# Performance work log

Hardware: AMD Instinct MI355X
Metric: run time of the kernel (lower is better)

Reference implementation:

```python
import jax, jax.numpy as jnp
import numpy as np

N_FILES = 256      # number of files (segments)
LINES = 128        # lines per file
T = N_FILES * LINES  # total lines = 32768
D_ENC = 768        # CodeBERT hidden size
HID = 256          # GCN hidden_dim
SD = 128           # shared_dim
PD = 128           # private_dim
WINDOW = 2         # line-graph window
S_AM = 30.0        # AM-Softmax scale
M_AM = 0.35        # AM-Softmax margin


def _build_edges():
    # build_line_graph: connect lines within a file at offsets 1..WINDOW, both directions
    idx = np.arange(T)
    srcs, dsts = [], []
    for off in range(1, WINDOW + 1):
        m = (idx % LINES) + off < LINES  # j stays inside the same file
        i = idx[m]; j = i + off
        srcs += [i, j]; dsts += [j, i]
    return np.stack([np.concatenate(srcs), np.concatenate(dsts)]).astype(np.int32)


def setup_inputs() -> dict:
    key = jax.random.key(0)
    ks = jax.random.split(key, 18)
    std = 0.02
    inp = {
        "line_emb": jax.random.normal(ks[0], (T, D_ENC), jnp.float32),
        "W1": jax.random.normal(ks[1], (D_ENC, HID), jnp.float32) * std,
        "b1": jnp.zeros((HID,), jnp.float32),
        "W2": jax.random.normal(ks[2], (HID, HID), jnp.float32) * std,
        "b2": jnp.zeros((HID,), jnp.float32),
        "attn_w": jax.random.normal(ks[3], (HID, 1), jnp.float32) * std,
        "attn_b": jnp.zeros((1,), jnp.float32),
        "Ws": jax.random.normal(ks[4], (HID, SD), jnp.float32) * std,
        "bs": jnp.zeros((SD,), jnp.float32),
        "Wp": jax.random.normal(ks[5], (HID, PD), jnp.float32) * std,
        "bp": jnp.zeros((PD,), jnp.float32),
        "cls_w": jax.random.normal(ks[6], (SD, 2), jnp.float32) * std,
        "Wd1": jax.random.normal(ks[7], (SD, SD), jnp.float32) * std,
        "bd1": jnp.zeros((SD,), jnp.float32),
        "Wd2": jax.random.normal(ks[8], (SD, 2), jnp.float32) * std,
        "bd2": jnp.zeros((2,), jnp.float32),
        "line_ptr": jnp.arange(0, T + 1, LINES, dtype=jnp.int32),
        "edge_index": jnp.asarray(_build_edges()),
        "file_labels": jax.random.randint(ks[9], (N_FILES,), 0, 2, jnp.int32),
    }
    return inp


def _l2norm(x):
    return x / jnp.maximum(jnp.linalg.norm(x, axis=1, keepdims=True), 1e-12)


def _gcn(x, W, b, src, dst, n):
    sl = jnp.arange(n, dtype=src.dtype)
    src = jnp.concatenate([src, sl]); dst = jnp.concatenate([dst, sl])
    deg = jax.ops.segment_sum(jnp.ones_like(src, jnp.float32), dst, num_segments=n)
    norm = jax.lax.rsqrt(deg[src] * deg[dst])  # [E+n]
    h = x @ W                                   # [n, out]
    msg = h[src] * norm[:, None]
    return jax.ops.segment_sum(msg, dst, num_segments=n) + b


def reference(line_emb, W1, b1, W2, b2, attn_w, attn_b, Ws, bs, Wp, bp,
              cls_w, Wd1, bd1, Wd2, bd2, line_ptr, edge_index, file_labels):
    n = line_emb.shape[0]
    n_files = line_ptr.shape[0] - 1
    src, dst = edge_index[0], edge_index[1]

    h = jax.nn.relu(_gcn(line_emb, W1, b1, src, dst, n))
    h = _gcn(h, W2, b2, src, dst, n)               # [T, HID]

    # ragged per-file softmax attention pooling
    seg = jnp.searchsorted(line_ptr, jnp.arange(n, dtype=line_ptr.dtype), side="right") - 1
    logits = (h @ attn_w).squeeze(-1) + attn_b[0]  # [T]
    seg_max = jax.ops.segment_max(logits, seg, num_segments=n_files)
    e = jnp.exp(logits - seg_max[seg])
    denom = jax.ops.segment_sum(e, seg, num_segments=n_files)
    att_weights = e / denom[seg]
    h_file = jax.ops.segment_sum(att_weights[:, None] * h, seg, num_segments=n_files)  # [N, HID]

    # disentangle heads
    z_shared = h_file @ Ws + bs
    z_private = h_file @ Wp + bp

    # AM-Softmax classifier (labels given -> subtract margin on true class)
    cos = _l2norm(z_shared) @ (cls_w / jnp.maximum(jnp.linalg.norm(cls_w, axis=0, keepdims=True), 1e-12))
    onehot = jax.nn.one_hot(file_labels, 2, dtype=cos.dtype)
    logits_cls = S_AM * (cos - M_AM * onehot)

    # orthogonality loss
    corr = _l2norm(z_shared).T @ _l2norm(z_private)
    ortho = jnp.linalg.norm(corr)

    # domain discriminator (GRL is identity in forward)
    domain_logits = jax.nn.relu(z_shared @ Wd1 + bd1) @ Wd2 + bd2

    return (logits_cls, h_file, z_shared, z_private, att_weights, domain_logits, ortho)
```

## Files before the change

kernel.cpp:

```cpp
#include <hip/hip_runtime.h>


typedef __attribute__((ext_vector_type(8))) short bf16x8;
typedef __attribute__((ext_vector_type(4))) short bf16x4;
typedef __attribute__((ext_vector_type(4))) float f32x4;
typedef __attribute__((ext_vector_type(8))) float f32x8;

__device__ __forceinline__ unsigned short f2bf(float f) {
  union { float f; unsigned int i; } v; v.f = f;
  unsigned int r = v.i + 0x7FFFu + ((v.i >> 16) & 1u);
  return (unsigned short)(r >> 16);
}
__device__ __forceinline__ int degf(int p) {
  return 5 - (p < 2 ? 2 - p : 0) - (p > 125 ? p - 125 : 0);
}

__global__ void cvt_transpose_tiled(const float* __restrict__ src,
                                    unsigned short* __restrict__ dst, int R, int C) {
  __shared__ float tile[32][33];
  int bx = blockIdx.x * 32, by = blockIdx.y * 32;
  int tx = threadIdx.x, ty = threadIdx.y;
#pragma unroll
  for (int j = 0; j < 32; j += 8)
    tile[ty + j][tx] = src[(by + ty + j) * C + bx + tx];
  __syncthreads();
#pragma unroll
  for (int j = 0; j < 32; j += 8)
    dst[(bx + ty + j) * R + by + tx] = f2bf(tile[tx][ty + j]);
}

__global__ __launch_bounds__(1024) void fused_gcn1(const float* __restrict__ A,
                                                   const unsigned short* __restrict__ Bt,
                                                   const float* __restrict__ bias,
                                                   unsigned short* __restrict__ G1) {
  __shared__ __align__(16) char lds[131072];
  unsigned short* sA = (unsigned short*)lds;
  unsigned short* sB = (unsigned short*)(lds + 32768);
  float* hL = (float*)lds;
  const int t = threadIdx.x;
  const int wave = t >> 6, lane = t & 63;
  const int wr = wave >> 2, wc = wave & 3;
  const long rowA = (long)blockIdx.x * 128;

  f32x4 acc[2][4];
#pragma unroll
  for (int m = 0; m < 2; ++m)
#pragma unroll
    for (int n = 0; n < 4; ++n) acc[m][n] = (f32x4)0.0f;

  const int arow = t >> 3, acol = (t & 7) * 8;
  const int aswz = arow * 64 + (acol ^ ((arow & 7) << 3));
  const int NKT = 12;
  f32x8 areg;

#define ISSUE_A1(kt) areg = *(const f32x8*)&A[(rowA + arow) * 768 + (kt) * 64 + acol]
#define WRITE_A1(buf) { unsigned short u[8];                                      \
    _Pragma("unroll") for (int j = 0; j < 8; ++j) u[j] = f2bf(areg[j]);           \
    *(bf16x8*)&sA[(buf) * 8192 + aswz] = *(bf16x8*)u; }
#define ISSUE_B1(kt, buf) _Pragma("unroll") for (int it = 0; it < 2; ++it) {      \
    int flat = (it * 1024 + t) * 8;                                               \
    int n = flat >> 6, k = flat & 63;                                             \
    const unsigned short* g = Bt + n * 768 + (kt) * 64 + (k ^ ((n & 7) << 3));    \
    __builtin_amdgcn_global_load_lds(                                             \
        (const __attribute__((address_space(1))) unsigned int*)g,                 \
        (__attribute__((address_space(3))) unsigned int*)                         \
            &sB[(buf) * 16384 + (it * 16 + wave) * 512], 16, 0, 0); }

  ISSUE_A1(0); ISSUE_B1(0, 0); WRITE_A1(0);
  __syncthreads();
  for (int kt = 0; kt < NKT; ++kt) {
    const int cur = kt & 1, nxt = cur ^ 1;
    if (kt + 1 < NKT) { ISSUE_A1(kt + 1); ISSUE_B1(kt + 1, nxt); }
#pragma unroll
    for (int kk = 0; kk < 2; ++kk) {
      const int kb = kk * 32 + (lane >> 4) * 8;
      bf16x8 af[2], bfr[4];
#pragma unroll
      for (int m = 0; m < 2; ++m) {
        int r = wr * 32 + m * 16 + (lane & 15);
        af[m] = *(const bf16x8*)&sA[cur * 8192 + r * 64 + (kb ^ ((r & 7) << 3))];
      }
#pragma unroll
      for (int n = 0; n < 4; ++n) {
        int r = wc * 64 + n * 16 + (lane & 15);
        bfr[n] = *(const bf16x8*)&sB[cur * 16384 + r * 64 + (kb ^ ((r & 7) << 3))];
      }
#pragma unroll
      for (int m = 0; m < 2; ++m)
#pragma unroll
        for (int n = 0; n < 4; ++n)
          acc[m][n] = __builtin_amdgcn_mfma_f32_16x16x32_bf16(af[m], bfr[n], acc[m][n], 0, 0, 0);
    }
    if (kt + 1 < NKT) WRITE_A1(nxt);
    __syncthreads();
  }
#pragma unroll
  for (int m = 0; m < 2; ++m)
#pragma unroll
    for (int n = 0; n < 4; ++n) {
      int r = wr * 32 + m * 16 + (lane >> 4) * 4;
      int c = wc * 64 + n * 16 + (lane & 15);
#pragma unroll
      for (int j = 0; j < 4; ++j) hL[(r + j) * 256 + c] = acc[m][n][j];
    }
  __syncthreads();
#pragma unroll
  for (int it = 0; it < 8; ++it) {
    int g = it * 1024 + t;
    int l = g >> 6, c0 = (g & 63) * 4;
    int dl = degf(l);
    f32x4 s = (f32x4)0.0f;
#pragma unroll
    for (int o = -2; o <= 2; ++o) {
      int q = l + o;
      if (q < 0 || q > 127) continue;
      float w = __frsqrt_rn((float)(dl * degf(q)));
      s += w * *(const f32x4*)&hL[q * 256 + c0];
    }
    f32x4 b = *(const f32x4*)&bias[c0];
    unsigned short o4[4];
#pragma unroll
    for (int j = 0; j < 4; ++j) o4[j] = f2bf(fmaxf(s[j] + b[j], 0.f));
    *(bf16x4*)&G1[(rowA + l) * 256 + c0] = *(bf16x4*)o4;
  }
#undef ISSUE_A1
#undef WRITE_A1
#undef ISSUE_B1
}

__global__ __launch_bounds__(1024) void fused_gcn2(const unsigned short* __restrict__ A,
                                                   const unsigned short* __restrict__ Bt,
                                                   const float* __restrict__ bias,
                                                   const float* __restrict__ attn_w,
                                                   const float* __restrict__ attn_b,
                                                   float* __restrict__ hf_ws,
                                                   float* __restrict__ out) {
  __shared__ __align__(16) char lds[131072];
  unsigned short* sA = (unsigned short*)lds;
  unsigned short* sB = (unsigned short*)(lds + 32768);
  float* hL = (float*)lds;
  __shared__ float awS[256];
  __shared__ float lgS[128];
  __shared__ float red[64];
  __shared__ float psum[4 * 256];
  const int t = threadIdx.x;
  const int wave = t >> 6, lane = t & 63;
  const int wr = wave >> 2, wc = wave & 3;
  const int file = blockIdx.x;
  const long rowA = (long)file * 128;

  if (t < 256) awS[t] = attn_w[t];

  f32x4 acc[2][4];
#pragma unroll
  for (int m = 0; m < 2; ++m)
#pragma unroll
    for (int n = 0; n < 4; ++n) acc[m][n] = (f32x4)0.0f;

  const int NKT = 4;

#define ISSUE_A2(kt, buf) {                                                       \
    int flat = t * 8;                                                             \
    int r = flat >> 6, k = flat & 63;                                             \
    const unsigned short* g = A + (rowA + r) * 256 + (kt) * 64 + (k ^ ((r & 7) << 3)); \
    __builtin_amdgcn_global_load_lds(                                             \
        (const __attribute__((address_space(1))) unsigned int*)g,                 \
        (__attribute__((address_space(3))) unsigned int*)                         \
            &sA[(buf) * 8192 + wave * 512], 16, 0, 0); }
#define ISSUE_B2(kt, buf) _Pragma("unroll") for (int it = 0; it < 2; ++it) {      \
    int flat = (it * 1024 + t) * 8;                                               \
    int n = flat >> 6, k = flat & 63;                                             \
    const unsigned short* g = Bt + n * 256 + (kt) * 64 + (k ^ ((n & 7) << 3));    \
    __builtin_amdgcn_global_load_lds(                                             \
        (const __attribute__((address_space(1))) unsigned int*)g,                 \
        (__attribute__((address_space(3))) unsigned int*)                         \
            &sB[(buf) * 16384 + (it * 16 + wave) * 512], 16, 0, 0); }

  ISSUE_A2(0, 0); ISSUE_B2(0, 0);
  __syncthreads();
  for (int kt = 0; kt < NKT; ++kt) {
    const int cur = kt & 1, nxt = cur ^ 1;
    if (kt + 1 < NKT) { ISSUE_A2(kt + 1, nxt); ISSUE_B2(kt + 1, nxt); }
#pragma unroll
    for (int kk = 0; kk < 2; ++kk) {
      const int kb = kk * 32 + (lane >> 4) * 8;
      bf16x8 af[2], bfr[4];
#pragma unroll
      for (int m = 0; m < 2; ++m) {
        int r = wr * 32 + m * 16 + (lane & 15);
        af[m] = *(const bf16x8*)&sA[cur * 8192 + r * 64 + (kb ^ ((r & 7) << 3))];
      }
#pragma unroll
      for (int n = 0; n < 4; ++n) {
        int r = wc * 64 + n * 16 + (lane & 15);
        bfr[n] = *(const bf16x8*)&sB[cur * 16384 + r * 64 + (kb ^ ((r & 7) << 3))];
      }
#pragma unroll
      for (int m = 0; m < 2; ++m)
#pragma unroll
        for (int n = 0; n < 4; ++n)
          acc[m][n] = __builtin_amdgcn_mfma_f32_16x16x32_bf16(af[m], bfr[n], acc[m][n], 0, 0, 0);
    }
    __syncthreads();
  }
#pragma unroll
  for (int m = 0; m < 2; ++m)
#pragma unroll
    for (int n = 0; n < 4; ++n) {
      int r = wr * 32 + m * 16 + (lane >> 4) * 4;
      int c = wc * 64 + n * 16 + (lane & 15);
#pragma unroll
      for (int j = 0; j < 4; ++j) hL[(r + j) * 256 + c] = acc[m][n][j];
    }
  __syncthreads();
  f32x4 st[2];
#pragma unroll
  for (int it = 0; it < 2; ++it) {
    int g = it * 1024 + t;
    int l = g >> 6, c0 = (g & 63) * 4;
    int dl = degf(l);
    f32x4 s = (f32x4)0.0f;
#pragma unroll
    for (int o = -2; o <= 2; ++o) {
      int q = l + o;
      if (q < 0 || q > 127) continue;
      float w = __frsqrt_rn((float)(dl * degf(q)));
      s += w * *(const f32x4*)&hL[q * 256 + c0];
    }
    f32x4 b = *(const f32x4*)&bias[c0];
    st[it] = s + b;
  }
  __syncthreads();
#pragma unroll
  for (int it = 0; it < 2; ++it) {
    int g = it * 1024 + t;
    int l = g >> 6, c0 = (g & 63) * 4;
    *(f32x4*)&hL[l * 256 + c0] = st[it];
  }
  __syncthreads();
  {
    int l = t >> 3, p = t & 7;
    float part = 0.f;
#pragma unroll 4
    for (int j = 0; j < 32; ++j) {
      int c = p * 32 + ((j + 4 * p + l) & 31);
      part += hL[l * 256 + c] * awS[c];
    }
    part += __shfl_xor(part, 1);
    part += __shfl_xor(part, 2);
    part += __shfl_xor(part, 4);
    if (p == 0) lgS[l] = part + attn_b[0];
  }
  __syncthreads();
  if (t < 64) red[t] = fmaxf(lgS[t], lgS[t + 64]);
  __syncthreads();
  for (int s = 32; s > 0; s >>= 1) {
    if (t < s) red[t] = fmaxf(red[t], red[t + s]);
    __syncthreads();
  }
  float mx = red[0];
  __syncthreads();
  if (t < 128) lgS[t] = expf(lgS[t] - mx);
  __syncthreads();
  if (t < 64) red[t] = lgS[t] + lgS[t + 64];
  __syncthreads();
  for (int s = 32; s > 0; s >>= 1) {
    if (t < s) red[t] += red[t + s];
    __syncthreads();
  }
  float dn = red[0];
  __syncthreads();
  if (t < 128) {
    float w = lgS[t] / dn;
    lgS[t] = w;
    out[131584 + file * 128 + t] = w;
  }
  __syncthreads();
  {
    int c = t & 255, grp = t >> 8;
    float s = 0.f;
    for (int l = grp * 32; l < grp * 32 + 32; ++l) s += lgS[l] * hL[l * 256 + c];
    psum[grp * 256 + c] = s;
  }
  __syncthreads();
  if (t < 256) {
    float tot = psum[t] + psum[256 + t] + psum[512 + t] + psum[768 + t];
    hf_ws[file * 256 + t] = tot;
    out[512 + file * 256 + t] = tot;
  }
#undef ISSUE_A2
#undef ISSUE_B2
}

__global__ __launch_bounds__(128) void head_kernel(const float* __restrict__ hf_ws,
    const float* __restrict__ Ws, const float* __restrict__ bs,
    const float* __restrict__ Wp, const float* __restrict__ bp,
    const float* __restrict__ cls_w, const int* __restrict__ labels,
    const float* __restrict__ Wd1, const float* __restrict__ bd1,
    const float* __restrict__ Wd2, const float* __restrict__ bd2,
    float* __restrict__ zsn_ws, float* __restrict__ zpn_ws,
    float* __restrict__ out) {
  const int f = blockIdx.x, j = threadIdx.x;
  __shared__ float hf[256];
  __shared__ float zsS[128];
  __shared__ float red[128];
  hf[j] = hf_ws[f * 256 + j];
  hf[j + 128] = hf_ws[f * 256 + 128 + j];
  __syncthreads();
  float zs = bs[j], zp = bp[j];
  for (int c = 0; c < 256; ++c) {
    float hv = hf[c];
    zs += hv * Ws[c * 128 + j];
    zp += hv * Wp[c * 128 + j];
  }
  out[66048 + f * 128 + j] = zs;
  out[98816 + f * 128 + j] = zp;
  zsS[j] = zs;
  red[j] = zs * zs; __syncthreads();
  for (int s = 64; s > 0; s >>= 1) { if (j < s) red[j] += red[j + s]; __syncthreads(); }
  float ns = sqrtf(red[0]); __syncthreads();
  float zsn = zs / fmaxf(ns, 1e-12f);
  zsn_ws[f * 128 + j] = zsn;
  red[j] = zp * zp; __syncthreads();
  for (int s = 64; s > 0; s >>= 1) { if (j < s) red[j] += red[j + s]; __syncthreads(); }
  float npn = sqrtf(red[0]); __syncthreads();
  zpn_ws[f * 128 + j] = zp / fmaxf(npn, 1e-12f);
  float c0 = 0.f, c1 = 0.f;
#pragma unroll
  for (int k = 0; k < 2; ++k) {
    float cw = cls_w[j * 2 + k];
    red[j] = zsn * cw; __syncthreads();
    for (int s = 64; s > 0; s >>= 1) { if (j < s) red[j] += red[j + s]; __syncthreads(); }
    float dk = red[0]; __syncthreads();
    red[j] = cw * cw; __syncthreads();
    for (int s = 64; s > 0; s >>= 1) { if (j < s) red[j] += red[j + s]; __syncthreads(); }
    float nk = sqrtf(red[0]); __syncthreads();
    float cosv = dk / fmaxf(nk, 1e-12f);
    if (k == 0) c0 = cosv; else c1 = cosv;
  }
  if (j < 2) {
    int lab = labels[f];
    float cv = (j == 0) ? c0 : c1;
    out[f * 2 + j] = 30.0f * (cv - 0.35f * (lab == j ? 1.f : 0.f));
  }
  float dd = bd1[j];
  for (int a = 0; a < 128; ++a) dd += zsS[a] * Wd1[a * 128 + j];
  dd = fmaxf(dd, 0.f);
#pragma unroll
  for (int k = 0; k < 2; ++k) {
    red[j] = dd * Wd2[j * 2 + k]; __syncthreads();
    for (int s = 64; s > 0; s >>= 1) { if (j < s) red[j] += red[j + s]; __syncthreads(); }
    if (j == 0) out[164352 + f * 2 + k] = red[0] + bd2[k];
    __syncthreads();
  }
}

__global__ __launch_bounds__(128) void ortho_partial(const float* __restrict__ zsn,
                                                     const float* __restrict__ zpn,
                                                     float* __restrict__ partial) {
  const int a = blockIdx.x, b = threadIdx.x;
  float s = 0.f;
  for (int f = 0; f < 256; ++f) s += zsn[f * 128 + a] * zpn[f * 128 + b];
  __shared__ float red[128];
  red[b] = s * s; __syncthreads();
  for (int st = 64; st > 0; st >>= 1) { if (b < st) red[b] += red[b + st]; __syncthreads(); }
  if (b == 0) partial[a] = red[0];
}

__global__ __launch_bounds__(128) void ortho_final(const float* __restrict__ partial,
                                                   float* __restrict__ out) {
  const int t = threadIdx.x;
  __shared__ float red[128];
  red[t] = partial[t]; __syncthreads();
  for (int st = 64; st > 0; st >>= 1) { if (t < st) red[t] += red[t + st]; __syncthreads(); }
  if (t == 0) out[164864] = sqrtf(red[0]);
}

extern "C" void kernel_launch(void* const* d_in, const int* in_sizes, int n_in,
                              void* d_out, int out_size, void* d_ws, size_t ws_size,
                              hipStream_t stream) {
  const float* line_emb = (const float*)d_in[0];
  const float* W1     = (const float*)d_in[1];
  const float* b1     = (const float*)d_in[2];
  const float* W2     = (const float*)d_in[3];
  const float* b2     = (const float*)d_in[4];
  const float* attn_w = (const float*)d_in[5];
  const float* attn_b = (const float*)d_in[6];
  const float* Ws     = (const float*)d_in[7];
  const float* bs     = (const float*)d_in[8];
  const float* Wp     = (const float*)d_in[9];
  const float* bp     = (const float*)d_in[10];
  const float* cls_w  = (const float*)d_in[11];
  const float* Wd1    = (const float*)d_in[12];
  const float* bd1    = (const float*)d_in[13];
  const float* Wd2    = (const float*)d_in[14];
  const float* bd2    = (const float*)d_in[15];
  const int* labels   = (const int*)d_in[18];

  char* ws = (char*)d_ws;
  unsigned short* W1t = (unsigned short*)(ws + 0);
  unsigned short* W2t = (unsigned short*)(ws + 393216);
  unsigned short* G1  = (unsigned short*)(ws + 524288);
  float* hf           = (float*)(ws + 17301504);
  float* zsn          = (float*)(ws + 17563648);
  float* zpn          = (float*)(ws + 17694720);
  float* partial      = (float*)(ws + 17825792);
  float* out          = (float*)d_out;

  cvt_transpose_tiled<<<dim3(8, 24), dim3(32, 8), 0, stream>>>(W1, W1t, 768, 256);
  cvt_transpose_tiled<<<dim3(8, 8), dim3(32, 8), 0, stream>>>(W2, W2t, 256, 256);
  fused_gcn1<<<dim3(256), dim3(1024), 0, stream>>>(line_emb, W1t, b1, G1);
  fused_gcn2<<<dim3(256), dim3(1024), 0, stream>>>(G1, W2t, b2, attn_w, attn_b, hf, out);
  head_kernel<<<dim3(256), dim3(128), 0, stream>>>(hf, Ws, bs, Wp, bp, cls_w, labels,
                                                   Wd1, bd1, Wd2, bd2, zsn, zpn, out);
  ortho_partial<<<dim3(128), dim3(128), 0, stream>>>(zsn, zpn, partial);
  ortho_final<<<dim3(1), dim3(128), 0, stream>>>(partial, out);
}
```

Before: 82.80 us.

## Fuse both GCN layers, pooling and heads into one per-file kernel

Merges the two transpose launches into one prep kernel, and fuses GCN layer 1, GCN layer 2, attention pooling and the per-file heads into one kernel per file. The layer-1 output now stays in LDS as bf16 instead of going through global memory. Pre-aggregation GEMM outputs are stored as bf16 in LDS to fit the buffers, which adds extra rounding. The head reductions use wave shuffles instead of chains of shared-memory tree reductions. This removes kernel launches and a global round trip of the intermediate activations, in exchange for higher LDS pressure and slightly lower precision.

```diff
diff --git a/kernel.cpp b/kernel.cpp
--- a/kernel.cpp
+++ b/kernel.cpp
@@ -11,14 +11,30 @@
   unsigned int r = v.i + 0x7FFFu + ((v.i >> 16) & 1u);
   return (unsigned short)(r >> 16);
 }
+__device__ __forceinline__ float bf2f(unsigned short u) {
+  union { unsigned int i; float f; } v; v.i = ((unsigned int)u) << 16; return v.f;
+}
+__device__ __forceinline__ float cvt4dot(bf16x4 v, f32x4* o) {
+  (*o)[0] = bf2f(((unsigned short*)&v)[0]); (*o)[1] = bf2f(((unsigned short*)&v)[1]);
+  (*o)[2] = bf2f(((unsigned short*)&v)[2]); (*o)[3] = bf2f(((unsigned short*)&v)[3]);
+  return 0.f;
+}
 __device__ __forceinline__ int degf(int p) {
   return 5 - (p < 2 ? 2 - p : 0) - (p > 125 ? p - 125 : 0);
 }
-
-__global__ void cvt_transpose_tiled(const float* __restrict__ src,
-                                    unsigned short* __restrict__ dst, int R, int C) {
+__device__ __forceinline__ float wsum(float v) {
+#pragma unroll
+  for (int o = 1; o < 64; o <<= 1) v += __shfl_xor(v, o);
+  return v;
+}
+
+__global__ void prep_weights(const float* __restrict__ W1, const float* __restrict__ W2,
+                             unsigned short* __restrict__ W1t, unsigned short* __restrict__ W2t) {
   __shared__ float tile[32][33];
-  int bx = blockIdx.x * 32, by = blockIdx.y * 32;
+  int id = blockIdx.x;
+  const float* src; unsigned short* dst; int R, C, bx, by;
+  if (id < 192) { src = W1; dst = W1t; R = 768; C = 256; bx = (id % 8) * 32; by = (id / 8) * 32; }
+  else { id -= 192; src = W2; dst = W2t; R = 256; C = 256; bx = (id % 8) * 32; by = (id / 8) * 32; }
   int tx = threadIdx.x, ty = threadIdx.y;
 #pragma unroll
   for (int j = 0; j < 32; j += 8)
@@ -29,18 +45,39 @@
     dst[(bx + ty + j) * R + by + tx] = f2bf(tile[tx][ty + j]);
 }
 
-__global__ __launch_bounds__(1024) void fused_gcn1(const float* __restrict__ A,
-                                                   const unsigned short* __restrict__ Bt,
-                                                   const float* __restrict__ bias,
-                                                   unsigned short* __restrict__ G1) {
+__global__ __launch_bounds__(1024) void mega(const float* __restrict__ A,
+    const unsigned short* __restrict__ W1t, const float* __restrict__ b1,
+    const unsigned short* __restrict__ W2t, const float* __restrict__ b2,
+    const float* __restrict__ attn_w, const float* __restrict__ attn_b,
+    const float* __restrict__ Ws, const float* __restrict__ bs,
+    const float* __restrict__ Wp, const float* __restrict__ bp,
+    const float* __restrict__ cls_w, const int* __restrict__ labels,
+    const float* __restrict__ Wd1, const float* __restrict__ bd1,
+    const float* __restrict__ Wd2, const float* __restrict__ bd2,
+    float* __restrict__ out) {
   __shared__ __align__(16) char lds[131072];
-  unsigned short* sA = (unsigned short*)lds;
-  unsigned short* sB = (unsigned short*)(lds + 32768);
-  float* hL = (float*)lds;
+  unsigned short* sA1 = (unsigned short*)lds;
+  unsigned short* sB1 = (unsigned short*)(lds + 32768);
+  unsigned short* H1  = (unsigned short*)lds;
+  unsigned short* G1L = (unsigned short*)(lds + 65536);
+  unsigned short* sB2 = (unsigned short*)lds;
+  unsigned short* H2  = (unsigned short*)lds;
+  unsigned short* hB  = (unsigned short*)(lds + 65536);
+  __shared__ float awS[256];
+  __shared__ float lgS[128];
+  __shared__ float redM[64];
+  __shared__ float scr[1024];
+  __shared__ float hfS[256];
+  __shared__ float zsS[128], znS[128];
+  __shared__ float redS[16];
+
   const int t = threadIdx.x;
   const int wave = t >> 6, lane = t & 63;
   const int wr = wave >> 2, wc = wave & 3;
-  const long rowA = (long)blockIdx.x * 128;
+  const int file = blockIdx.x;
+  const long rowA = (long)file * 128;
+
+  if (t < 256) awS[t] = attn_w[t];
 
   f32x4 acc[2][4];
 #pragma unroll
@@ -50,27 +87,25 @@
 
   const int arow = t >> 3, acol = (t & 7) * 8;
   const int aswz = arow * 64 + (acol ^ ((arow & 7) << 3));
-  const int NKT = 12;
   f32x8 areg;
-
 #define ISSUE_A1(kt) areg = *(const f32x8*)&A[(rowA + arow) * 768 + (kt) * 64 + acol]
 #define WRITE_A1(buf) { unsigned short u[8];                                      \
     _Pragma("unroll") for (int j = 0; j < 8; ++j) u[j] = f2bf(areg[j]);           \
-    *(bf16x8*)&sA[(buf) * 8192 + aswz] = *(bf16x8*)u; }
+    *(bf16x8*)&sA1[(buf) * 8192 + aswz] = *(bf16x8*)u; }
 #define ISSUE_B1(kt, buf) _Pragma("unroll") for (int it = 0; it < 2; ++it) {      \
     int flat = (it * 1024 + t) * 8;                                               \
     int n = flat >> 6, k = flat & 63;                                             \
-    const unsigned short* g = Bt + n * 768 + (kt) * 64 + (k ^ ((n & 7) << 3));    \
+    const unsigned short* g = W1t + n * 768 + (kt) * 64 + (k ^ ((n & 7) << 3));   \
     __builtin_amdgcn_global_load_lds(                                             \
         (const __attribute__((address_space(1))) unsigned int*)g,                 \
         (__attribute__((address_space(3))) unsigned int*)                         \
-            &sB[(buf) * 16384 + (it * 16 + wave) * 512], 16, 0, 0); }
+            &sB1[(buf) * 16384 + (it * 16 + wave) * 512], 16, 0, 0); }
 
   ISSUE_A1(0); ISSUE_B1(0, 0); WRITE_A1(0);
   __syncthreads();
-  for (int kt = 0; kt < NKT; ++kt) {
+  for (int kt = 0; kt < 12; ++kt) {
     const int cur = kt & 1, nxt = cur ^ 1;
-    if (kt + 1 < NKT) { ISSUE_A1(kt + 1); ISSUE_B1(kt + 1, nxt); }
+    if (kt + 1 < 12) { ISSUE_A1(kt + 1); ISSUE_B1(kt + 1, nxt); }
 #pragma unroll
     for (int kk = 0; kk < 2; ++kk) {
       const int kb = kk * 32 + (lane >> 4) * 8;
@@ -78,12 +113,12 @@
 #pragma unroll
       for (int m = 0; m < 2; ++m) {
         int r = wr * 32 + m * 16 + (lane & 15);
-        af[m] = *(const bf16x8*)&sA[cur * 8192 + r * 64 + (kb ^ ((r & 7) << 3))];
+        af[m] = *(const bf16x8*)&sA1[cur * 8192 + r * 64 + (kb ^ ((r & 7) << 3))];
       }
 #pragma unroll
       for (int n = 0; n < 4; ++n) {
         int r = wc * 64 + n * 16 + (lane & 15);
-        bfr[n] = *(const bf16x8*)&sB[cur * 16384 + r * 64 + (kb ^ ((r & 7) << 3))];
+        bfr[n] = *(const bf16x8*)&sB1[cur * 16384 + r * 64 + (kb ^ ((r & 7) << 3))];
       }
 #pragma unroll
       for (int m = 0; m < 2; ++m)
@@ -91,7 +126,7 @@
         for (int n = 0; n < 4; ++n)
           acc[m][n] = __builtin_amdgcn_mfma_f32_16x16x32_bf16(af[m], bfr[n], acc[m][n], 0, 0, 0);
     }
-    if (kt + 1 < NKT) WRITE_A1(nxt);
+    if (kt + 1 < 12) WRITE_A1(nxt);
     __syncthreads();
   }
 #pragma unroll
@@ -101,7 +136,7 @@
       int r = wr * 32 + m * 16 + (lane >> 4) * 4;
       int c = wc * 64 + n * 16 + (lane & 15);
 #pragma unroll
-      for (int j = 0; j < 4; ++j) hL[(r + j) * 256 + c] = acc[m][n][j];
+      for (int j = 0; j < 4; ++j) H1[(r + j) * 256 + c] = f2bf(acc[m][n][j]);
     }
   __syncthreads();
 #pragma unroll
@@ -115,72 +150,36 @@
       int q = l + o;
       if (q < 0 || q > 127) continue;
       float w = __frsqrt_rn((float)(dl * degf(q)));
-      s += w * *(const f32x4*)&hL[q * 256 + c0];
-    }
-    f32x4 b = *(const f32x4*)&bias[c0];
+      bf16x4 hv4 = *(const bf16x4*)&H1[q * 256 + c0];
+      f32x4 hv; cvt4dot(hv4, &hv);
+      s += w * hv;
+    }
+    f32x4 b = *(const f32x4*)&b1[c0];
     unsigned short o4[4];
 #pragma unroll
     for (int j = 0; j < 4; ++j) o4[j] = f2bf(fmaxf(s[j] + b[j], 0.f));
-    *(bf16x4*)&G1[(rowA + l) * 256 + c0] = *(bf16x4*)o4;
-  }
-#undef ISSUE_A1
-#undef WRITE_A1
-#undef ISSUE_B1
-}
-
-__global__ __launch_bounds__(1024) void fused_gcn2(const unsigned short* __restrict__ A,
-                                                   const unsigned short* __restrict__ Bt,
-                                                   const float* __restrict__ bias,
-                                                   const float* __restrict__ attn_w,
-                                                   const float* __restrict__ attn_b,
-                                                   float* __restrict__ hf_ws,
-                                                   float* __restrict__ out) {
-  __shared__ __align__(16) char lds[131072];
-  unsigned short* sA = (unsigned short*)lds;
-  unsigned short* sB = (unsigned short*)(lds + 32768);
-  float* hL = (float*)lds;
-  __shared__ float awS[256];
-  __shared__ float lgS[128];
-  __shared__ float red[64];
-  __shared__ float psum[4 * 256];
-  const int t = threadIdx.x;
-  const int wave = t >> 6, lane = t & 63;
-  const int wr = wave >> 2, wc = wave & 3;
-  const int file = blockIdx.x;
-  const long rowA = (long)file * 128;
-
-  if (t < 256) awS[t] = attn_w[t];
-
-  f32x4 acc[2][4];
+    *(bf16x4*)&G1L[l * 256 + (c0 ^ ((l & 7) << 3))] = *(bf16x4*)o4;
+  }
+  __syncthreads();
+
 #pragma unroll
   for (int m = 0; m < 2; ++m)
 #pragma unroll
     for (int n = 0; n < 4; ++n) acc[m][n] = (f32x4)0.0f;
-
-  const int NKT = 4;
-
-#define ISSUE_A2(kt, buf) {                                                       \
-    int flat = t * 8;                                                             \
-    int r = flat >> 6, k = flat & 63;                                             \
-    const unsigned short* g = A + (rowA + r) * 256 + (kt) * 64 + (k ^ ((r & 7) << 3)); \
+#define ISSUE_B2(kt, buf) _Pragma("unroll") for (int it = 0; it < 2; ++it) {      \
+    int flat = (it * 1024 + t) * 8;                                               \
+    int n = flat >> 6, k = flat & 63;                                             \
+    const unsigned short* g = W2t + n * 256 + (kt) * 64 + (k ^ ((n & 7) << 3));   \
     __builtin_amdgcn_global_load_lds(                                             \
         (const __attribute__((address_space(1))) unsigned int*)g,                 \
         (__attribute__((address_space(3))) unsigned int*)                         \
-            &sA[(buf) * 8192 + wave * 512], 16, 0, 0); }
-#define ISSUE_B2(kt, buf) _Pragma("unroll") for (int it = 0; it < 2; ++it) {      \
-    int flat = (it * 1024 + t) * 8;                                               \
-    int n = flat >> 6, k = flat & 63;                                             \
-    const unsigned short* g = Bt + n * 256 + (kt) * 64 + (k ^ ((n & 7) << 3));    \
-    __builtin_amdgcn_global_load_lds(                                             \
-        (const __attribute__((address_space(1))) unsigned int*)g,                 \
-        (__attribute__((address_space(3))) unsigned int*)                         \
-            &sB[(buf) * 16384 + (it * 16 + wave) * 512], 16, 0, 0); }
-
-  ISSUE_A2(0, 0); ISSUE_B2(0, 0);
-  __syncthreads();
-  for (int kt = 0; kt < NKT; ++kt) {
+            &sB2[(buf) * 16384 + (it * 16 + wave) * 512], 16, 0, 0); }
+
+  ISSUE_B2(0, 0);
+  __syncthreads();
+  for (int kt = 0; kt < 4; ++kt) {
     const int cur = kt & 1, nxt = cur ^ 1;
-    if (kt + 1 < NKT) { ISSUE_A2(kt + 1, nxt); ISSUE_B2(kt + 1, nxt); }
+    if (kt + 1 < 4) ISSUE_B2(kt + 1, nxt);
 #pragma unroll
     for (int kk = 0; kk < 2; ++kk) {
       const int kb = kk * 32 + (lane >> 4) * 8;
@@ -188,12 +187,13 @@
 #pragma unroll
       for (int m = 0; m < 2; ++m) {
         int r = wr * 32 + m * 16 + (lane & 15);
-        af[m] = *(const bf16x8*)&sA[cur * 8192 + r * 64 + (kb ^ ((r & 7) << 3))];
+        int col = kt * 64 + kb;
+        af[m] = *(const bf16x8*)&G1L[r * 256 + (col ^ ((r & 7) << 3))];
       }
 #pragma unroll
       for (int n = 0; n < 4; ++n) {
         int r = wc * 64 + n * 16 + (lane & 15);
-        bfr[n] = *(const bf16x8*)&sB[cur * 16384 + r * 64 + (kb ^ ((r & 7) << 3))];
+        bfr[n] = *(const bf16x8*)&sB2[cur * 16384 + r * 64 + (kb ^ ((r & 7) << 3))];
       }
 #pragma unroll
       for (int m = 0; m < 2; ++m)
@@ -210,12 +210,11 @@
       int r = wr * 32 + m * 16 + (lane >> 4) * 4;
       int c = wc * 64 + n * 16 + (lane & 15);
 #pragma unroll
-      for (int j = 0; j < 4; ++j) hL[(r + j) * 256 + c] = acc[m][n][j];
-    }
-  __syncthreads();
-  f32x4 st[2];
-#pragma unroll
-  for (int it = 0; it < 2; ++it) {
+      for (int j = 0; j < 4; ++j) H2[(r + j) * 256 + c] = f2bf(acc[m][n][j]);
+    }
+  __syncthreads();
+#pragma unroll
+  for (int it = 0; it < 8; ++it) {
     int g = it * 1024 + t;
     int l = g >> 6, c0 = (g & 63) * 4;
     int dl = degf(l);
@@ -225,26 +224,25 @@
       int q = l + o;
       if (q < 0 || q > 127) continue;
       float w = __frsqrt_rn((float)(dl * degf(q)));
-      s += w * *(const f32x4*)&hL[q * 256 + c0];
-    }
-    f32x4 b = *(const f32x4*)&bias[c0];
-    st[it] = s + b;
-  }
-  __syncthreads();
-#pragma unroll
-  for (int it = 0; it < 2; ++it) {
-    int g = it * 1024 + t;
-    int l = g >> 6, c0 = (g & 63) * 4;
-    *(f32x4*)&hL[l * 256 + c0] = st[it];
-  }
-  __syncthreads();
+      bf16x4 hv4 = *(const bf16x4*)&H2[q * 256 + c0];
+      f32x4 hv; cvt4dot(hv4, &hv);
+      s += w * hv;
+    }
+    f32x4 b = *(const f32x4*)&b2[c0];
+    unsigned short o4[4];
+#pragma unroll
+    for (int j = 0; j < 4; ++j) o4[j] = f2bf(s[j] + b[j]);
+    *(bf16x4*)&hB[l * 256 + c0] = *(bf16x4*)o4;
+  }
+  __syncthreads();
+
   {
     int l = t >> 3, p = t & 7;
     float part = 0.f;
 #pragma unroll 4
     for (int j = 0; j < 32; ++j) {
       int c = p * 32 + ((j + 4 * p + l) & 31);
-      part += hL[l * 256 + c] * awS[c];
+      part += bf2f(hB[l * 256 + c]) * awS[c];
     }
     part += __shfl_xor(part, 1);
     part += __shfl_xor(part, 2);
@@ -252,23 +250,23 @@
     if (p == 0) lgS[l] = part + attn_b[0];
   }
   __syncthreads();
-  if (t < 64) red[t] = fmaxf(lgS[t], lgS[t + 64]);
+  if (t < 64) redM[t] = fmaxf(lgS[t], lgS[t + 64]);
   __syncthreads();
   for (int s = 32; s > 0; s >>= 1) {
-    if (t < s) red[t] = fmaxf(red[t], red[t + s]);
+    if (t < s) redM[t] = fmaxf(redM[t], redM[t + s]);
     __syncthreads();
   }
-  float mx = red[0];
+  float mx = redM[0];
   __syncthreads();
   if (t < 128) lgS[t] = expf(lgS[t] - mx);
   __syncthreads();
-  if (t < 64) red[t] = lgS[t] + lgS[t + 64];
+  if (t < 64) redM[t] = lgS[t] + lgS[t + 64];
   __syncthreads();
   for (int s = 32; s > 0; s >>= 1) {
-    if (t < s) red[t] += red[t + s];
+    if (t < s) redM[t] += redM[t + s];
     __syncthreads();
   }
-  float dn = red[0];
+  float dn = redM[0];
   __syncthreads();
   if (t < 128) {
     float w = lgS[t] / dn;
@@ -279,80 +277,109 @@
   {
     int c = t & 255, grp = t >> 8;
     float s = 0.f;
-    for (int l = grp * 32; l < grp * 32 + 32; ++l) s += lgS[l] * hL[l * 256 + c];
-    psum[grp * 256 + c] = s;
+    for (int l = grp * 32; l < grp * 32 + 32; ++l) s += lgS[l] * bf2f(hB[l * 256 + c]);
+    scr[grp * 256 + c] = s;
   }
   __syncthreads();
   if (t < 256) {
-    float tot = psum[t] + psum[256 + t] + psum[512 + t] + psum[768 + t];
-    hf_ws[file * 256 + t] = tot;
+    float tot = scr[t] + scr[256 + t] + scr[512 + t] + scr[768 + t];
+    hfS[t] = tot;
     out[512 + file * 256 + t] = tot;
   }
-#undef ISSUE_A2
+  __syncthreads();
+
+  {
+    if (t < 512) {
+      int g = t >> 7, j = t & 127;
+      float s = 0.f;
+      for (int c = g * 64; c < g * 64 + 64; ++c) s += hfS[c] * Ws[c * 128 + j];
+      scr[g * 128 + j] = s;
+    } else {
+      int tt = t - 512, g = tt >> 7, j = tt & 127;
+      float s = 0.f;
+      for (int c = g * 64; c < g * 64 + 64; ++c) s += hfS[c] * Wp[c * 128 + j];
+      scr[512 + g * 128 + j] = s;
+    }
+  }
+  __syncthreads();
+  {
+    int j = t & 127;
+    if (t < 128) {
+      float zs = bs[j] + scr[j] + scr[128 + j] + scr[256 + j] + scr[384 + j];
+      zsS[j] = zs;
+      out[66048 + file * 128 + j] = zs;
+      float s = wsum(zs * zs);
+      if (lane == 0) redS[wave] = s;
+    } else if (t < 256) {
+      float zp = bp[j] + scr[512 + j] + scr[640 + j] + scr[768 + j] + scr[896 + j];
+      out[98816 + file * 128 + j] = zp;
+    }
+  }
+  __syncthreads();
+  if (t == 0) redS[8] = fmaxf(sqrtf(redS[0] + redS[1]), 1e-12f);
+  __syncthreads();
+  if (t < 128) znS[t] = zsS[t] / redS[8];
+  __syncthreads();
+  {
+    int j = t & 127;
+    if (t < 512) {
+      float v;
+      if (t < 128)       v = znS[j] * cls_w[j * 2 + 0];
+      else if (t < 256)  v = znS[j] * cls_w[j * 2 + 1];
+      else if (t < 384)  { float w0 = cls_w[j * 2 + 0]; v = w0 * w0; }
+      else               { float w1 = cls_w[j * 2 + 1]; v = w1 * w1; }
+      float s = wsum(v);
+      if (lane == 0) redS[wave] = s;
+    }
+  }
+  __syncthreads();
+  if (t == 0) {
+    float d0 = redS[0] + redS[1], d1 = redS[2] + redS[3];
+    float n0 = fmaxf(sqrtf(redS[4] + redS[5]), 1e-12f);
+    float n1 = fmaxf(sqrtf(redS[6] + redS[7]), 1e-12f);
+    int lab = labels[file];
+    out[file * 2 + 0] = 30.0f * (d0 / n0 - 0.35f * (lab == 0 ? 1.f : 0.f));
+    out[file * 2 + 1] = 30.0f * (d1 / n1 - 0.35f * (lab == 1 ? 1.f : 0.f));
+  }
+  __syncthreads();
+  {
+    int j = t & 127;
+    if (t < 128) {
+      float dd = bd1[j];
+      for (int a = 0; a < 128; ++a) dd += zsS[a] * Wd1[a * 128 + j];
+      dd = fmaxf(dd, 0.f);
+      float s0 = wsum(dd * Wd2[j * 2 + 0]);
+      if (lane == 0) redS[wave] = s0;
+      float s1 = wsum(dd * Wd2[j * 2 + 1]);
+      if (lane == 0) redS[4 + wave] = s1;
+    }
+  }
+  __syncthreads();
+  if (t == 0) {
+    out[164352 + file * 2 + 0] = redS[0] + redS[1] + bd2[0];
+    out[164352 + file * 2 + 1] = redS[4] + redS[5] + bd2[1];
+  }
+#undef ISSUE_A1
+#undef WRITE_A1
+#undef ISSUE_B1
 #undef ISSUE_B2
 }
 
-__global__ __launch_bounds__(128) void head_kernel(const float* __restrict__ hf_ws,
-    const float* __restrict__ Ws, const float* __restrict__ bs,
-    const float* __restrict__ Wp, const float* __restrict__ bp,
-    const float* __restrict__ cls_w, const int* __restrict__ labels,
-    const float* __restrict__ Wd1, const float* __restrict__ bd1,
-    const float* __restrict__ Wd2, const float* __restrict__ bd2,
-    float* __restrict__ zsn_ws, float* __restrict__ zpn_ws,
-    float* __restrict__ out) {
+__global__ __launch_bounds__(128) void znorm(const float* __restrict__ out,
+                                             float* __restrict__ zsn,
+                                             float* __restrict__ zpn) {
   const int f = blockIdx.x, j = threadIdx.x;
-  __shared__ float hf[256];
-  __shared__ float zsS[128];
   __shared__ float red[128];
-  hf[j] = hf_ws[f * 256 + j];
-  hf[j + 128] = hf_ws[f * 256 + 128 + j];
-  __syncthreads();
-  float zs = bs[j], zp = bp[j];
-  for (int c = 0; c < 256; ++c) {
-    float hv = hf[c];
-    zs += hv * Ws[c * 128 + j];
-    zp += hv * Wp[c * 128 + j];
-  }
-  out[66048 + f * 128 + j] = zs;
-  out[98816 + f * 128 + j] = zp;
-  zsS[j] = zs;
+  float zs = out[66048 + f * 128 + j];
+  float zp = out[98816 + f * 128 + j];
   red[j] = zs * zs; __syncthreads();
   for (int s = 64; s > 0; s >>= 1) { if (j < s) red[j] += red[j + s]; __syncthreads(); }
   float ns = sqrtf(red[0]); __syncthreads();
-  float zsn = zs / fmaxf(ns, 1e-12f);
-  zsn_ws[f * 128 + j] = zsn;
+  zsn[f * 128 + j] = zs / fmaxf(ns, 1e-12f);
   red[j] = zp * zp; __syncthreads();
   for (int s = 64; s > 0; s >>= 1) { if (j < s) red[j] += red[j + s]; __syncthreads(); }
-  float npn = sqrtf(red[0]); __syncthreads();
-  zpn_ws[f * 128 + j] = zp / fmaxf(npn, 1e-12f);
-  float c0 = 0.f, c1 = 0.f;
-#pragma unroll
-  for (int k = 0; k < 2; ++k) {
-    float cw = cls_w[j * 2 + k];
-    red[j] = zsn * cw; __syncthreads();
-    for (int s = 64; s > 0; s >>= 1) { if (j < s) red[j] += red[j + s]; __syncthreads(); }
-    float dk = red[0]; __syncthreads();
-    red[j] = cw * cw; __syncthreads();
-    for (int s = 64; s > 0; s >>= 1) { if (j < s) red[j] += red[j + s]; __syncthreads(); }
-    float nk = sqrtf(red[0]); __syncthreads();
-    float cosv = dk / fmaxf(nk, 1e-12f);
-    if (k == 0) c0 = cosv; else c1 = cosv;
-  }
-  if (j < 2) {
-    int lab = labels[f];
-    float cv = (j == 0) ? c0 : c1;
-    out[f * 2 + j] = 30.0f * (cv - 0.35f * (lab == j ? 1.f : 0.f));
-  }
-  float dd = bd1[j];
-  for (int a = 0; a < 128; ++a) dd += zsS[a] * Wd1[a * 128 + j];
-  dd = fmaxf(dd, 0.f);
-#pragma unroll
-  for (int k = 0; k < 2; ++k) {
-    red[j] = dd * Wd2[j * 2 + k]; __syncthreads();
-    for (int s = 64; s > 0; s >>= 1) { if (j < s) red[j] += red[j + s]; __syncthreads(); }
-    if (j == 0) out[164352 + f * 2 + k] = red[0] + bd2[k];
-    __syncthreads();
-  }
+  float np = sqrtf(red[0]); __syncthreads();
+  zpn[f * 128 + j] = zp / fmaxf(np, 1e-12f);
 }
 
 __global__ __launch_bounds__(128) void ortho_partial(const float* __restrict__ zsn,
@@ -400,19 +427,16 @@
   char* ws = (char*)d_ws;
   unsigned short* W1t = (unsigned short*)(ws + 0);
   unsigned short* W2t = (unsigned short*)(ws + 393216);
-  unsigned short* G1  = (unsigned short*)(ws + 524288);
-  float* hf           = (float*)(ws + 17301504);
-  float* zsn          = (float*)(ws + 17563648);
-  float* zpn          = (float*)(ws + 17694720);
-  float* partial      = (float*)(ws + 17825792);
+  float* zsn          = (float*)(ws + 524288);
+  float* zpn          = (float*)(ws + 655360);
+  float* partial      = (float*)(ws + 786432);
   float* out          = (float*)d_out;
 
-  cvt_transpose_tiled<<<dim3(8, 24), dim3(32, 8), 0, stream>>>(W1, W1t, 768, 256);
-  cvt_transpose_tiled<<<dim3(8, 8), dim3(32, 8), 0, stream>>>(W2, W2t, 256, 256);
-  fused_gcn1<<<dim3(256), dim3(1024), 0, stream>>>(line_emb, W1t, b1, G1);
-  fused_gcn2<<<dim3(256), dim3(1024), 0, stream>>>(G1, W2t, b2, attn_w, attn_b, hf, out);
-  head_kernel<<<dim3(256), dim3(128), 0, stream>>>(hf, Ws, bs, Wp, bp, cls_w, labels,
-                                                   Wd1, bd1, Wd2, bd2, zsn, zpn, out);
+  prep_weights<<<dim3(256), dim3(32, 8), 0, stream>>>(W1, W2, W1t, W2t);
+  mega<<<dim3(256), dim3(1024), 0, stream>>>(line_emb, W1t, b1, W2t, b2,
+                                             attn_w, attn_b, Ws, bs, Wp, bp,
+                                             cls_w, labels, Wd1, bd1, Wd2, bd2, out);
+  znorm<<<dim3(256), dim3(128), 0, stream>>>(out, zsn, zpn);
   ortho_partial<<<dim3(128), dim3(128), 0, stream>>>(zsn, zpn, partial);
   ortho_final<<<dim3(1), dim3(128), 0, stream>>>(partial, out);
 }
```

Measured after the change: 74.73 us. 1.11x faster.
